# Kernel optimization log

Hardware: AMD Instinct MI355X
Metric: run time of the kernel (lower is better)

## Reference

```python
import jax, jax.numpy as jnp
import numpy as np

B, T, D, H, HD = 4, 2048, 1024, 16, 64
EPS = 1e-6


def _rotary_tables(seq_len, d_head):
    n = d_head // 4
    angular_freq = (1.0 / 1024) ** jnp.linspace(0, 1, n, dtype=jnp.float32)
    angular_freq = jnp.concatenate([angular_freq, jnp.zeros((n,), jnp.float32)])  # [d_head//2]
    theta = jnp.outer(jnp.arange(seq_len, dtype=jnp.float32), angular_freq)  # [T, d_head//2]
    return jnp.cos(theta), jnp.sin(theta)


def _apply_rotary(x, cos, sin):
    # x: [B, T, H, d]
    xf = x.astype(jnp.float32)
    x1, x2 = jnp.split(xf, 2, axis=-1)
    c = cos[None, :, None, :]
    s = sin[None, :, None, :]
    y1 = x1 * c + x2 * s
    y2 = -x1 * s + x2 * c
    return jnp.concatenate([y1, y2], axis=-1).astype(x.dtype)


def _rmsnorm(x, eps):
    return x * jax.lax.rsqrt(jnp.mean(x * x, axis=-1, keepdims=True) + eps)


def setup_inputs() -> dict:
    key = jax.random.key(0)
    ks = jax.random.split(key, 5)
    scale = 1.0 / np.sqrt(D)
    x = jax.random.normal(ks[0], (B, T, D), jnp.float32)
    wq = jax.random.normal(ks[1], (D, D), jnp.float32) * scale
    wk = jax.random.normal(ks[2], (D, D), jnp.float32) * scale
    wv = jax.random.normal(ks[3], (D, D), jnp.float32) * scale
    wo = jax.random.normal(ks[4], (D, D), jnp.float32) * scale
    mask = jnp.tril(jnp.ones((T, T), dtype=bool))  # causal
    return {"x": x, "wq": wq, "wk": wk, "wv": wv, "wo": wo, "mask": mask}


def reference(x, wq, wk, wv, wo, mask):
    # QKV projections (equinox Linear: y = x @ W.T)
    q = (x @ wq.T).reshape(B, T, H, HD)
    k = (x @ wk.T).reshape(B, T, H, HD)
    v = (x @ wv.T).reshape(B, T, H, HD)
    # QK-norm (RMS norm without weight)
    q = _rmsnorm(q, EPS)
    k = _rmsnorm(k, EPS)
    # Rotary embedding
    cos, sin = _rotary_tables(T, HD)
    q = _apply_rotary(q, cos, sin)
    k = _apply_rotary(k, cos, sin)
    # Attention
    scores = jnp.einsum('bshd,bthd->bhst', q, k) / jnp.sqrt(jnp.float32(HD))
    scores = jnp.where(mask[None, None, :, :], scores, -jnp.inf)
    weights = jax.nn.softmax(scores, axis=-1)
    out = jnp.einsum('bhst,bthd->bshd', weights, v)
    out = out.reshape(B, T, D)
    return out @ wo.T
```

## Files before the change

### kernel.cpp

```cpp
#include <hip/hip_runtime.h>
#include <hip/hip_bf16.h>
#include <math.h>

#define B_ 4
#define T_ 2048
#define D_ 1024
#define H_ 16
#define HD_ 64

typedef _Float16 f16x8 __attribute__((ext_vector_type(8)));
typedef _Float16 f16x4 __attribute__((ext_vector_type(4)));
typedef float f32x4 __attribute__((ext_vector_type(4)));

__device__ __forceinline__ void gload_lds16(const _Float16* g, _Float16* l) {
    __builtin_amdgcn_global_load_lds(
        (const __attribute__((address_space(1))) void*)g,
        (__attribute__((address_space(3))) void*)l,
        16, 0, 0);
}

__global__ __launch_bounds__(256) void castf(const float* __restrict__ in,
                                             _Float16* __restrict__ out, int n4) {
    const int i = blockIdx.x * 256 + threadIdx.x;
    if (i < n4) {
        const float4 v = ((const float4*)in)[i];
        f16x4 h = {(_Float16)v.x, (_Float16)v.y, (_Float16)v.z, (_Float16)v.w};
        ((f16x4*)out)[i] = h;
    }
}

__global__ __launch_bounds__(256) void castw(const float* __restrict__ a,
                                             const float* __restrict__ b,
                                             const float* __restrict__ c,
                                             const float* __restrict__ d,
                                             _Float16* __restrict__ oa,
                                             _Float16* __restrict__ ob,
                                             _Float16* __restrict__ oc,
                                             _Float16* __restrict__ od) {
    const int z = blockIdx.z;
    const float* in = (z == 0) ? a : (z == 1 ? b : (z == 2 ? c : d));
    _Float16* out = (z == 0) ? oa : (z == 1 ? ob : (z == 2 ? oc : od));
    const int i = blockIdx.x * 256 + threadIdx.x;
    const float4 v = ((const float4*)in)[i];
    f16x4 h = {(_Float16)v.x, (_Float16)v.y, (_Float16)v.z, (_Float16)v.w};
    ((f16x4*)out)[i] = h;
}

__global__ __launch_bounds__(256) void gemm_qkv(const _Float16* __restrict__ A,
                                                const _Float16* __restrict__ Wq,
                                                const _Float16* __restrict__ Wk,
                                                const _Float16* __restrict__ Wv,
                                                _Float16* __restrict__ qh,
                                                _Float16* __restrict__ kh,
                                                _Float16* __restrict__ vt) {
    constexpr int K = D_;
    const int z = blockIdx.z;
    const _Float16* W = (z == 0) ? Wq : (z == 1 ? Wk : Wv);
    __shared__ _Float16 As[128 * 32];
    __shared__ _Float16 Bs[128 * 32];
    const int tid = threadIdx.x;
    const int lane = tid & 63, w = tid >> 6;
    const int col = lane & 15, quad = lane >> 4;
    const int wm = w >> 1, wn = w & 1;
    const int row0 = blockIdx.y * 128, col0 = blockIdx.x * 128;
    const int sr = lane >> 2, sc = (lane & 3) * 8;

    f32x4 acc[4][4];
#pragma unroll
    for (int i = 0; i < 4; ++i)
#pragma unroll
        for (int j = 0; j < 4; ++j) acc[i][j] = (f32x4){0.f, 0.f, 0.f, 0.f};

    for (int kt = 0; kt < K / 32; ++kt) {
        const int k0 = kt * 32;
#pragma unroll
        for (int it = 0; it < 2; ++it) {
            const int rb = it * 64 + w * 16;
            gload_lds16(A + (size_t)(row0 + rb + sr) * K + k0 + sc, As + rb * 32);
            gload_lds16(W + (size_t)(col0 + rb + sr) * K + k0 + sc, Bs + rb * 32);
        }
        __syncthreads();
        f16x8 af[4], bf[4];
#pragma unroll
        for (int i = 0; i < 4; ++i) {
            af[i] = *(const f16x8*)&As[(wm * 64 + i * 16 + col) * 32 + quad * 8];
            bf[i] = *(const f16x8*)&Bs[(wn * 64 + i * 16 + col) * 32 + quad * 8];
        }
#pragma unroll
        for (int mi = 0; mi < 4; ++mi)
#pragma unroll
            for (int ni = 0; ni < 4; ++ni)
                acc[mi][ni] = __builtin_amdgcn_mfma_f32_16x16x32_f16(af[mi], bf[ni],
                                                                     acc[mi][ni], 0, 0, 0);
        __syncthreads();
    }

    if (z < 2) {
        _Float16* C = (z == 0) ? qh : kh;
        const float qscale = (z == 0) ? 0.18033688011112042f : 1.0f;
        const float fr = exp2f(-10.0f * (float)col * (1.0f / 15.0f));
#pragma unroll
        for (int mi = 0; mi < 4; ++mi) {
            float ssq[4];
#pragma unroll
            for (int r = 0; r < 4; ++r) {
                float t = 0.f;
#pragma unroll
                for (int ni = 0; ni < 4; ++ni) t += acc[mi][ni][r] * acc[mi][ni][r];
                ssq[r] = t;
            }
#pragma unroll
            for (int st = 1; st < 16; st <<= 1)
#pragma unroll
                for (int r = 0; r < 4; ++r) ssq[r] += __shfl_xor(ssq[r], st, 64);
            const int rowb = row0 + wm * 64 + mi * 16 + quad * 4;
#pragma unroll
            for (int r = 0; r < 4; ++r) {
                const float scl = rsqrtf(ssq[r] * (1.0f / 64.0f) + 1e-6f) * qscale;
                const int t = (rowb + r) & (T_ - 1);
                float s, c;
                sincosf((float)t * fr, &s, &c);
                const float x0 = acc[mi][0][r] * scl;
                const float x1 = acc[mi][1][r] * scl;
                const float x2 = acc[mi][2][r] * scl;
                const float x3 = acc[mi][3][r] * scl;
                const float y0 = fmaf(x0, c, x2 * s);
                const float y2 = fmaf(x2, c, -x0 * s);
                const size_t base = (size_t)(rowb + r) * D_ + col0 + wn * 64 + col;
                C[base + 0]  = (_Float16)y0;
                C[base + 16] = (_Float16)x1;
                C[base + 32] = (_Float16)y2;
                C[base + 48] = (_Float16)x3;
            }
        }
    } else {
        const int hh = blockIdx.x * 2 + wn;
#pragma unroll
        for (int mi = 0; mi < 4; ++mi) {
            const int row = row0 + wm * 64 + mi * 16 + quad * 4;
            const int bb = row >> 11;
            const int t0m = row & (T_ - 1);
#pragma unroll
            for (int ni = 0; ni < 4; ++ni) {
                const int d = ni * 16 + col;
                f16x4 pk = {(_Float16)acc[mi][ni][0], (_Float16)acc[mi][ni][1],
                            (_Float16)acc[mi][ni][2], (_Float16)acc[mi][ni][3]};
                *(f16x4*)&vt[((size_t)(bb * H_ + hh) * HD_ + d) * T_ + t0m] = pk;
            }
        }
    }
}

__global__ __launch_bounds__(256) void gemm_wo(const _Float16* __restrict__ A,
                                               const _Float16* __restrict__ W,
                                               float* __restrict__ C) {
    constexpr int K = D_, N = D_;
    __shared__ _Float16 As[128 * 32];
    __shared__ _Float16 Bs[128 * 32];
    const int tid = threadIdx.x;
    const int lane = tid & 63, w = tid >> 6;
    const int col = lane & 15, quad = lane >> 4;
    const int wm = w >> 1, wn = w & 1;
    const int row0 = blockIdx.y * 128, col0 = blockIdx.x * 128;
    const int sr = lane >> 2, sc = (lane & 3) * 8;

    f32x4 acc[4][4];
#pragma unroll
    for (int i = 0; i < 4; ++i)
#pragma unroll
        for (int j = 0; j < 4; ++j) acc[i][j] = (f32x4){0.f, 0.f, 0.f, 0.f};

    for (int kt = 0; kt < K / 32; ++kt) {
        const int k0 = kt * 32;
#pragma unroll
        for (int it = 0; it < 2; ++it) {
            const int rb = it * 64 + w * 16;
            gload_lds16(A + (size_t)(row0 + rb + sr) * K + k0 + sc, As + rb * 32);
            gload_lds16(W + (size_t)(col0 + rb + sr) * K + k0 + sc, Bs + rb * 32);
        }
        __syncthreads();
        f16x8 af[4], bf[4];
#pragma unroll
        for (int i = 0; i < 4; ++i) {
            af[i] = *(const f16x8*)&As[(wm * 64 + i * 16 + col) * 32 + quad * 8];
            bf[i] = *(const f16x8*)&Bs[(wn * 64 + i * 16 + col) * 32 + quad * 8];
        }
#pragma unroll
        for (int mi = 0; mi < 4; ++mi)
#pragma unroll
            for (int ni = 0; ni < 4; ++ni)
                acc[mi][ni] = __builtin_amdgcn_mfma_f32_16x16x32_f16(af[mi], bf[ni],
                                                                     acc[mi][ni], 0, 0, 0);
        __syncthreads();
    }
#pragma unroll
    for (int mi = 0; mi < 4; ++mi)
#pragma unroll
        for (int ni = 0; ni < 4; ++ni)
#pragma unroll
            for (int r = 0; r < 4; ++r)
                C[(size_t)(row0 + wm * 64 + mi * 16 + quad * 4 + r) * N +
                  col0 + wn * 64 + ni * 16 + col] = acc[mi][ni][r];
}

#define LDP 88

__global__ __launch_bounds__(512) void flash_mfma(const _Float16* __restrict__ qh,
                                                  const _Float16* __restrict__ kh,
                                                  const _Float16* __restrict__ vt,
                                                  _Float16* __restrict__ o) {
    __shared__ _Float16 Kl[64 * 64];
    __shared__ _Float16 Vl[64 * 64];
    __shared__ _Float16 Pl[8][16 * LDP];
    const int tid = threadIdx.x;
    const int lane = tid & 63, w = tid >> 6;
    const int col = lane & 15, quad = lane >> 4;
    const int bh = blockIdx.x, b = bh >> 4, h = bh & 15;
    const int srow = lane >> 3;
    const int schunk = (lane & 7) ^ srow;
    const int sw = col & 7;

    for (int phase = 0; phase < 2; ++phase) {
        const int qt = (phase == 0) ? (int)blockIdx.y : (15 - (int)blockIdx.y);
        const int q0 = qt * 128;

        const int tq = q0 + w * 16 + col;
        const _Float16* qp = qh + ((size_t)(b * T_ + tq) * H_ + h) * HD_ + quad * 8;
        const f16x8 qB0 = *(const f16x8*)(qp);
        const f16x8 qB1 = *(const f16x8*)(qp + 32);

        f32x4 oa[4];
#pragma unroll
        for (int i = 0; i < 4; ++i) oa[i] = (f32x4){0.f, 0.f, 0.f, 0.f};
        float l_ = 0.f;

        const int nkt = 2 * qt + 2;
        for (int kt = 0; kt < nkt; ++kt) {
            const int k0 = kt * 64;
            {
                const int r = w * 8 + srow;
                gload_lds16(kh + ((size_t)(b * T_ + k0 + r) * H_ + h) * HD_ + schunk * 8,
                            Kl + (w * 8) * 64);
                gload_lds16(vt + ((size_t)(b * H_ + h) * HD_ + r) * T_ + k0 + schunk * 8,
                            Vl + (w * 8) * 64);
            }
            __syncthreads();

            f32x4 s[4];
#pragma unroll
            for (int tn = 0; tn < 4; ++tn) {
                const _Float16* kp = &Kl[(tn * 16 + col) * 64];
                const f16x8 kA0 = *(const f16x8*)(kp + ((quad ^ sw) << 3));
                const f16x8 kA1 = *(const f16x8*)(kp + (((quad | 4) ^ sw) << 3));
                f32x4 a = (f32x4){0.f, 0.f, 0.f, 0.f};
                a = __builtin_amdgcn_mfma_f32_16x16x32_f16(kA0, qB0, a, 0, 0, 0);
                a = __builtin_amdgcn_mfma_f32_16x16x32_f16(kA1, qB1, a, 0, 0, 0);
                s[tn] = a;
            }

            if (k0 + 63 > q0 + w * 16) {
                const int qq = q0 + w * 16 + col;
#pragma unroll
                for (int tn = 0; tn < 4; ++tn)
#pragma unroll
                    for (int r = 0; r < 4; ++r) {
                        const int key = k0 + tn * 16 + quad * 4 + r;
                        if (key > qq) s[tn][r] = -1e30f;
                    }
            }

#pragma unroll
            for (int tn = 0; tn < 4; ++tn) {
                f16x4 pk;
#pragma unroll
                for (int r = 0; r < 4; ++r) {
                    const float p = exp2f(s[tn][r]);
                    l_ += p;
                    pk[r] = (_Float16)p;
                }
                *(f16x4*)&Pl[w][col * LDP + tn * 16 + quad * 4] = pk;
            }

            const f16x8 pA0 = *(const f16x8*)&Pl[w][col * LDP + quad * 8];
            const f16x8 pA1 = *(const f16x8*)&Pl[w][col * LDP + quad * 8 + 32];
#pragma unroll
            for (int tn = 0; tn < 4; ++tn) {
                const _Float16* vp = &Vl[(tn * 16 + col) * 64];
                const f16x8 vB0 = *(const f16x8*)(vp + ((quad ^ sw) << 3));
                const f16x8 vB1 = *(const f16x8*)(vp + (((quad | 4) ^ sw) << 3));
                oa[tn] = __builtin_amdgcn_mfma_f32_16x16x32_f16(pA0, vB0, oa[tn], 0, 0, 0);
                oa[tn] = __builtin_amdgcn_mfma_f32_16x16x32_f16(pA1, vB1, oa[tn], 0, 0, 0);
            }
            __syncthreads();
        }

        l_ += __shfl_xor(l_, 16, 64);
        l_ += __shfl_xor(l_, 32, 64);
        const float linv = 1.0f / l_;
        float inv[4];
#pragma unroll
        for (int r = 0; r < 4; ++r) inv[r] = __shfl(linv, quad * 4 + r, 64);
#pragma unroll
        for (int tn = 0; tn < 4; ++tn)
#pragma unroll
            for (int r = 0; r < 4; ++r)
                o[((size_t)(b * T_ + q0 + w * 16 + quad * 4 + r) * H_ + h) * HD_ + tn * 16 + col] =
                    (_Float16)(oa[tn][r] * inv[r]);
    }
}

extern "C" void kernel_launch(void* const* d_in, const int* in_sizes, int n_in,
                              void* d_out, int out_size, void* d_ws, size_t ws_size,
                              hipStream_t stream) {
    const float* x  = (const float*)d_in[0];
    const float* wq = (const float*)d_in[1];
    const float* wk = (const float*)d_in[2];
    const float* wv = (const float*)d_in[3];
    const float* wo = (const float*)d_in[4];
    float* out = (float*)d_out;

    const size_t NE = (size_t)B_ * T_ * D_;
    const size_t WE = (size_t)D_ * D_;
    _Float16* xh  = (_Float16*)d_ws;
    _Float16* qh  = xh + NE;
    _Float16* kh  = qh + NE;
    _Float16* vth = kh + NE;
    _Float16* oh  = vth + NE;
    _Float16* wqh = oh + NE;
    _Float16* wkh = wqh + WE;
    _Float16* wvh = wkh + WE;
    _Float16* woh = wvh + WE;

    castf<<<NE / 1024, 256, 0, stream>>>(x, xh, (int)(NE / 4));
    castw<<<dim3(WE / 1024, 1, 4), 256, 0, stream>>>(wq, wk, wv, wo,
                                                     wqh, wkh, wvh, woh);

    gemm_qkv<<<dim3(D_ / 128, (B_ * T_) / 128, 3), 256, 0, stream>>>(
        xh, wqh, wkh, wvh, qh, kh, vth);

    flash_mfma<<<dim3(B_ * H_, 8, 1), 512, 0, stream>>>(qh, kh, vth, oh);

    gemm_wo<<<dim3(D_ / 128, (B_ * T_) / 128, 1), 256, 0, stream>>>(oh, woh, out);
}
```

Before: 279.4 us.

## Double-buffer K/V tiles in flash attention and swap GEMM grid axes

```diff
diff --git a/kernel.cpp b/kernel.cpp
--- a/kernel.cpp
+++ b/kernel.cpp
@@ -62,7 +62,7 @@
     const int lane = tid & 63, w = tid >> 6;
     const int col = lane & 15, quad = lane >> 4;
     const int wm = w >> 1, wn = w & 1;
-    const int row0 = blockIdx.y * 128, col0 = blockIdx.x * 128;
+    const int row0 = blockIdx.x * 128, col0 = blockIdx.y * 128;
     const int sr = lane >> 2, sc = (lane & 3) * 8;
 
     f32x4 acc[4][4];
@@ -119,7 +119,7 @@
                 const float scl = rsqrtf(ssq[r] * (1.0f / 64.0f) + 1e-6f) * qscale;
                 const int t = (rowb + r) & (T_ - 1);
                 float s, c;
-                sincosf((float)t * fr, &s, &c);
+                __sincosf((float)t * fr, &s, &c);
                 const float x0 = acc[mi][0][r] * scl;
                 const float x1 = acc[mi][1][r] * scl;
                 const float x2 = acc[mi][2][r] * scl;
@@ -134,7 +134,7 @@
             }
         }
     } else {
-        const int hh = blockIdx.x * 2 + wn;
+        const int hh = blockIdx.y * 2 + wn;
 #pragma unroll
         for (int mi = 0; mi < 4; ++mi) {
             const int row = row0 + wm * 64 + mi * 16 + quad * 4;
@@ -161,7 +161,7 @@
     const int lane = tid & 63, w = tid >> 6;
     const int col = lane & 15, quad = lane >> 4;
     const int wm = w >> 1, wn = w & 1;
-    const int row0 = blockIdx.y * 128, col0 = blockIdx.x * 128;
+    const int row0 = blockIdx.x * 128, col0 = blockIdx.y * 128;
     const int sr = lane >> 2, sc = (lane & 3) * 8;
 
     f32x4 acc[4][4];
@@ -209,8 +209,8 @@
                                                   const _Float16* __restrict__ kh,
                                                   const _Float16* __restrict__ vt,
                                                   _Float16* __restrict__ o) {
-    __shared__ _Float16 Kl[64 * 64];
-    __shared__ _Float16 Vl[64 * 64];
+    __shared__ _Float16 Kl[2][64 * 64];
+    __shared__ _Float16 Vl[2][64 * 64];
     __shared__ _Float16 Pl[8][16 * LDP];
     const int tid = threadIdx.x;
     const int lane = tid & 63, w = tid >> 6;
@@ -219,6 +219,9 @@
     const int srow = lane >> 3;
     const int schunk = (lane & 7) ^ srow;
     const int sw = col & 7;
+    const int sr = w * 8 + srow;
+    const _Float16* kbase = kh + ((size_t)(b * T_ + sr) * H_ + h) * HD_ + schunk * 8;
+    const _Float16* vbase = vt + ((size_t)(b * H_ + h) * HD_ + sr) * T_ + schunk * 8;
 
     for (int phase = 0; phase < 2; ++phase) {
         const int qt = (phase == 0) ? (int)blockIdx.y : (15 - (int)blockIdx.y);
@@ -235,21 +238,23 @@
         float l_ = 0.f;
 
         const int nkt = 2 * qt + 2;
+        gload_lds16(kbase, Kl[0] + (w * 8) * 64);
+        gload_lds16(vbase, Vl[0] + (w * 8) * 64);
+
         for (int kt = 0; kt < nkt; ++kt) {
+            const int cur = kt & 1;
+            __syncthreads();
+            if (kt + 1 < nkt) {
+                const int k1 = (kt + 1) * 64;
+                gload_lds16(kbase + (size_t)k1 * D_, Kl[cur ^ 1] + (w * 8) * 64);
+                gload_lds16(vbase + k1, Vl[cur ^ 1] + (w * 8) * 64);
+            }
             const int k0 = kt * 64;
-            {
-                const int r = w * 8 + srow;
-                gload_lds16(kh + ((size_t)(b * T_ + k0 + r) * H_ + h) * HD_ + schunk * 8,
-                            Kl + (w * 8) * 64);
-                gload_lds16(vt + ((size_t)(b * H_ + h) * HD_ + r) * T_ + k0 + schunk * 8,
-                            Vl + (w * 8) * 64);
-            }
-            __syncthreads();
 
             f32x4 s[4];
 #pragma unroll
             for (int tn = 0; tn < 4; ++tn) {
-                const _Float16* kp = &Kl[(tn * 16 + col) * 64];
+                const _Float16* kp = &Kl[cur][(tn * 16 + col) * 64];
                 const f16x8 kA0 = *(const f16x8*)(kp + ((quad ^ sw) << 3));
                 const f16x8 kA1 = *(const f16x8*)(kp + (((quad | 4) ^ sw) << 3));
                 f32x4 a = (f32x4){0.f, 0.f, 0.f, 0.f};
@@ -285,14 +290,14 @@
             const f16x8 pA1 = *(const f16x8*)&Pl[w][col * LDP + quad * 8 + 32];
 #pragma unroll
             for (int tn = 0; tn < 4; ++tn) {
-                const _Float16* vp = &Vl[(tn * 16 + col) * 64];
+                const _Float16* vp = &Vl[cur][(tn * 16 + col) * 64];
                 const f16x8 vB0 = *(const f16x8*)(vp + ((quad ^ sw) << 3));
                 const f16x8 vB1 = *(const f16x8*)(vp + (((quad | 4) ^ sw) << 3));
                 oa[tn] = __builtin_amdgcn_mfma_f32_16x16x32_f16(pA0, vB0, oa[tn], 0, 0, 0);
                 oa[tn] = __builtin_amdgcn_mfma_f32_16x16x32_f16(pA1, vB1, oa[tn], 0, 0, 0);
             }
-            __syncthreads();
-        }
+        }
+        __syncthreads();
 
         l_ += __shfl_xor(l_, 16, 64);
         l_ += __shfl_xor(l_, 32, 64);
@@ -335,10 +340,10 @@
     castw<<<dim3(WE / 1024, 1, 4), 256, 0, stream>>>(wq, wk, wv, wo,
                                                      wqh, wkh, wvh, woh);
 
-    gemm_qkv<<<dim3(D_ / 128, (B_ * T_) / 128, 3), 256, 0, stream>>>(
+    gemm_qkv<<<dim3((B_ * T_) / 128, D_ / 128, 3), 256, 0, stream>>>(
         xh, wqh, wkh, wvh, qh, kh, vth);
 
     flash_mfma<<<dim3(B_ * H_, 8, 1), 512, 0, stream>>>(qh, kh, vth, oh);
 
-    gemm_wo<<<dim3(D_ / 128, (B_ * T_) / 128, 1), 256, 0, stream>>>(oh, woh, out);
-}
+    gemm_wo<<<dim3((B_ * T_) / 128, D_ / 128, 1), 256, 0, stream>>>(oh, woh, out);
+}
```

Result: no change. 280.5 us (+0.4%).

## Double-buffer LDS tiles in projection GEMMs and swap grid tile order

Applied to the files above, without the earlier changes.

```diff
diff --git a/kernel.cpp b/kernel.cpp
--- a/kernel.cpp
+++ b/kernel.cpp
@@ -56,14 +56,16 @@
     constexpr int K = D_;
     const int z = blockIdx.z;
     const _Float16* W = (z == 0) ? Wq : (z == 1 ? Wk : Wv);
-    __shared__ _Float16 As[128 * 32];
-    __shared__ _Float16 Bs[128 * 32];
+    __shared__ _Float16 As[2][128 * 32];
+    __shared__ _Float16 Bs[2][128 * 32];
     const int tid = threadIdx.x;
     const int lane = tid & 63, w = tid >> 6;
     const int col = lane & 15, quad = lane >> 4;
     const int wm = w >> 1, wn = w & 1;
-    const int row0 = blockIdx.y * 128, col0 = blockIdx.x * 128;
+    const int row0 = blockIdx.x * 128, col0 = blockIdx.y * 128;
     const int sr = lane >> 2, sc = (lane & 3) * 8;
+    const _Float16* abase = A + (size_t)(row0 + sr) * K + sc;
+    const _Float16* wbase = W + (size_t)(col0 + sr) * K + sc;
 
     f32x4 acc[4][4];
 #pragma unroll
@@ -71,20 +73,30 @@
 #pragma unroll
         for (int j = 0; j < 4; ++j) acc[i][j] = (f32x4){0.f, 0.f, 0.f, 0.f};
 
+#pragma unroll
+    for (int it = 0; it < 2; ++it) {
+        const int rb = it * 64 + w * 16;
+        gload_lds16(abase + (size_t)rb * K, As[0] + rb * 32);
+        gload_lds16(wbase + (size_t)rb * K, Bs[0] + rb * 32);
+    }
+
     for (int kt = 0; kt < K / 32; ++kt) {
-        const int k0 = kt * 32;
-#pragma unroll
-        for (int it = 0; it < 2; ++it) {
-            const int rb = it * 64 + w * 16;
-            gload_lds16(A + (size_t)(row0 + rb + sr) * K + k0 + sc, As + rb * 32);
-            gload_lds16(W + (size_t)(col0 + rb + sr) * K + k0 + sc, Bs + rb * 32);
-        }
+        const int cur = kt & 1;
         __syncthreads();
+        if (kt + 1 < K / 32) {
+            const int k1 = (kt + 1) * 32;
+#pragma unroll
+            for (int it = 0; it < 2; ++it) {
+                const int rb = it * 64 + w * 16;
+                gload_lds16(abase + (size_t)rb * K + k1, As[cur ^ 1] + rb * 32);
+                gload_lds16(wbase + (size_t)rb * K + k1, Bs[cur ^ 1] + rb * 32);
+            }
+        }
         f16x8 af[4], bf[4];
 #pragma unroll
         for (int i = 0; i < 4; ++i) {
-            af[i] = *(const f16x8*)&As[(wm * 64 + i * 16 + col) * 32 + quad * 8];
-            bf[i] = *(const f16x8*)&Bs[(wn * 64 + i * 16 + col) * 32 + quad * 8];
+            af[i] = *(const f16x8*)&As[cur][(wm * 64 + i * 16 + col) * 32 + quad * 8];
+            bf[i] = *(const f16x8*)&Bs[cur][(wn * 64 + i * 16 + col) * 32 + quad * 8];
         }
 #pragma unroll
         for (int mi = 0; mi < 4; ++mi)
@@ -92,7 +104,6 @@
             for (int ni = 0; ni < 4; ++ni)
                 acc[mi][ni] = __builtin_amdgcn_mfma_f32_16x16x32_f16(af[mi], bf[ni],
                                                                      acc[mi][ni], 0, 0, 0);
-        __syncthreads();
     }
 
     if (z < 2) {
@@ -119,7 +130,7 @@
                 const float scl = rsqrtf(ssq[r] * (1.0f / 64.0f) + 1e-6f) * qscale;
                 const int t = (rowb + r) & (T_ - 1);
                 float s, c;
-                sincosf((float)t * fr, &s, &c);
+                __sincosf((float)t * fr, &s, &c);
                 const float x0 = acc[mi][0][r] * scl;
                 const float x1 = acc[mi][1][r] * scl;
                 const float x2 = acc[mi][2][r] * scl;
@@ -134,7 +145,7 @@
             }
         }
     } else {
-        const int hh = blockIdx.x * 2 + wn;
+        const int hh = blockIdx.y * 2 + wn;
 #pragma unroll
         for (int mi = 0; mi < 4; ++mi) {
             const int row = row0 + wm * 64 + mi * 16 + quad * 4;
@@ -155,14 +166,16 @@
                                                const _Float16* __restrict__ W,
                                                float* __restrict__ C) {
     constexpr int K = D_, N = D_;
-    __shared__ _Float16 As[128 * 32];
-    __shared__ _Float16 Bs[128 * 32];
+    __shared__ _Float16 As[2][128 * 32];
+    __shared__ _Float16 Bs[2][128 * 32];
     const int tid = threadIdx.x;
     const int lane = tid & 63, w = tid >> 6;
     const int col = lane & 15, quad = lane >> 4;
     const int wm = w >> 1, wn = w & 1;
-    const int row0 = blockIdx.y * 128, col0 = blockIdx.x * 128;
+    const int row0 = blockIdx.x * 128, col0 = blockIdx.y * 128;
     const int sr = lane >> 2, sc = (lane & 3) * 8;
+    const _Float16* abase = A + (size_t)(row0 + sr) * K + sc;
+    const _Float16* wbase = W + (size_t)(col0 + sr) * K + sc;
 
     f32x4 acc[4][4];
 #pragma unroll
@@ -170,20 +183,30 @@
 #pragma unroll
         for (int j = 0; j < 4; ++j) acc[i][j] = (f32x4){0.f, 0.f, 0.f, 0.f};
 
+#pragma unroll
+    for (int it = 0; it < 2; ++it) {
+        const int rb = it * 64 + w * 16;
+        gload_lds16(abase + (size_t)rb * K, As[0] + rb * 32);
+        gload_lds16(wbase + (size_t)rb * K, Bs[0] + rb * 32);
+    }
+
     for (int kt = 0; kt < K / 32; ++kt) {
-        const int k0 = kt * 32;
-#pragma unroll
-        for (int it = 0; it < 2; ++it) {
-            const int rb = it * 64 + w * 16;
-            gload_lds16(A + (size_t)(row0 + rb + sr) * K + k0 + sc, As + rb * 32);
-            gload_lds16(W + (size_t)(col0 + rb + sr) * K + k0 + sc, Bs + rb * 32);
-        }
+        const int cur = kt & 1;
         __syncthreads();
+        if (kt + 1 < K / 32) {
+            const int k1 = (kt + 1) * 32;
+#pragma unroll
+            for (int it = 0; it < 2; ++it) {
+                const int rb = it * 64 + w * 16;
+                gload_lds16(abase + (size_t)rb * K + k1, As[cur ^ 1] + rb * 32);
+                gload_lds16(wbase + (size_t)rb * K + k1, Bs[cur ^ 1] + rb * 32);
+            }
+        }
         f16x8 af[4], bf[4];
 #pragma unroll
         for (int i = 0; i < 4; ++i) {
-            af[i] = *(const f16x8*)&As[(wm * 64 + i * 16 + col) * 32 + quad * 8];
-            bf[i] = *(const f16x8*)&Bs[(wn * 64 + i * 16 + col) * 32 + quad * 8];
+            af[i] = *(const f16x8*)&As[cur][(wm * 64 + i * 16 + col) * 32 + quad * 8];
+            bf[i] = *(const f16x8*)&Bs[cur][(wn * 64 + i * 16 + col) * 32 + quad * 8];
         }
 #pragma unroll
         for (int mi = 0; mi < 4; ++mi)
@@ -191,7 +214,6 @@
             for (int ni = 0; ni < 4; ++ni)
                 acc[mi][ni] = __builtin_amdgcn_mfma_f32_16x16x32_f16(af[mi], bf[ni],
                                                                      acc[mi][ni], 0, 0, 0);
-        __syncthreads();
     }
 #pragma unroll
     for (int mi = 0; mi < 4; ++mi)
@@ -335,10 +357,10 @@
     castw<<<dim3(WE / 1024, 1, 4), 256, 0, stream>>>(wq, wk, wv, wo,
                                                      wqh, wkh, wvh, woh);
 
-    gemm_qkv<<<dim3(D_ / 128, (B_ * T_) / 128, 3), 256, 0, stream>>>(
+    gemm_qkv<<<dim3((B_ * T_) / 128, D_ / 128, 3), 256, 0, stream>>>(
         xh, wqh, wkh, wvh, qh, kh, vth);
 
     flash_mfma<<<dim3(B_ * H_, 8, 1), 512, 0, stream>>>(qh, kh, vth, oh);
 
-    gemm_wo<<<dim3(D_ / 128, (B_ * T_) / 128, 1), 256, 0, stream>>>(oh, woh, out);
-}
+    gemm_wo<<<dim3((B_ * T_) / 128, D_ / 128, 1), 256, 0, stream>>>(oh, woh, out);
+}
```

Measured after the change: 286.1 us. 1.02x slower.
